# Kernel tuning notes

Hardware: AMD Instinct MI355X
Metric: run time of the kernel (lower is better)

The kernel has to match this reference:

```python
import jax, jax.numpy as jnp
import numpy as np

N = 128  # image size
J = 4    # number of scales
L = 4    # number of orientations


def make_morlet_filters(n, j_max, n_angles):
    """Fixed Morlet filter bank in Fourier space, shape [J, L, N, N] (real)."""
    freqs = np.fft.fftfreq(n) * 2.0 * np.pi
    kx = freqs[:, None] * np.ones((1, n))
    ky = np.ones((n, 1)) * freqs[None, :]
    filters = np.zeros((j_max, n_angles, n, n), dtype=np.float32)
    for j in range(j_max):
        k0 = 3.0 * np.pi / 4.0 / (2.0 ** j)   # central frequency of scale j
        sigma = 0.8 * (2.0 ** j)               # gaussian width in space
        for l in range(n_angles):
            theta = np.pi * l / n_angles
            k0x, k0y = k0 * np.cos(theta), k0 * np.sin(theta)
            beta = np.exp(-0.5 * sigma ** 2 * k0 ** 2)  # zero-mean correction
            g_shift = np.exp(-0.5 * sigma ** 2 * ((kx - k0x) ** 2 + (ky - k0y) ** 2))
            g_zero = np.exp(-0.5 * sigma ** 2 * (kx ** 2 + ky ** 2))
            filters[j, l] = g_shift - beta * g_zero
    return jnp.asarray(filters)


PSI = make_morlet_filters(N, J, L)  # fixed (non-learned) filter bank
VALID_PAIRS = [(j1, j2) for j1 in range(J) for j2 in range(J) if j2 > j1]  # 6 pairs


def setup_inputs() -> dict:
    key = jax.random.key(0)
    k1, k2, k3, k4, k5 = jax.random.split(key, 5)
    B = 64
    return {
        "image_batch": jax.random.normal(k1, (B, N, N), dtype=jnp.float32),
        "fc1_w": jax.random.normal(k2, (4, 11), dtype=jnp.float32) * 0.3,
        "fc1_b": jax.random.normal(k3, (4,), dtype=jnp.float32) * 0.1,
        "fc2_w": jax.random.normal(k4, (10, 4), dtype=jnp.float32) * 0.3,
        "fc2_b": jax.random.normal(k5, (10,), dtype=jnp.float32) * 0.1,
    }


def _scattering(image):
    # image: [B, N, N]
    i_hat = jnp.fft.fft2(image)  # [B,N,N] complex64
    s0 = jnp.mean(image, axis=(1, 2))  # [B]
    # first order: |x * psi_{j1,l1}|  -> [B,J,L,N,N]
    u1 = jnp.abs(jnp.fft.ifft2(i_hat[:, None, None] * PSI[None]))
    s1 = jnp.mean(u1, axis=(2, 3, 4))  # [B,J] averaged over orientations+space
    u1_hat = jnp.fft.fft2(u1)  # [B,J,L,N,N]
    # second order: only j2 > j1 (others NaN in original and masked out)
    s2_list = []
    for (j1, j2) in VALID_PAIRS:
        # [B, L1, L2, N, N]
        field = jnp.fft.ifft2(u1_hat[:, j1, :, None] * PSI[j2][None, None])
        s2_list.append(jnp.mean(jnp.abs(field), axis=(1, 2, 3, 4)))
    s2 = jnp.stack(s2_list, axis=1)  # [B,6]
    return jnp.concatenate([s0[:, None], s1, s2], axis=1)  # [B,11]


def reference(image_batch, fc1_w, fc1_b, fc2_w, fc2_b):
    coeffs = _scattering(image_batch)                      # [B,11]
    h = jax.nn.relu(coeffs @ fc1_w.T + fc1_b)              # [B,4]
    return jax.nn.sigmoid(h @ fc2_w.T + fc2_b)             # [B,10]
```

## Files before the change

### kernel.cpp

```cpp
#include <hip/hip_runtime.h>
#include <math.h>

#define NN   128
#define SS   129
#define TT   512
#define NPIX 16384
#define EPT  32
#define SG   65
#define SG32 33


__device__ __forceinline__ float2 cmul(float2 a, float2 w) {
    return make_float2(a.x * w.x - a.y * w.y, a.x * w.y + a.y * w.x);
}
__device__ __forceinline__ float2 cmulc(float2 a, float2 w) {
    return make_float2(a.x * w.x + a.y * w.y, a.y * w.x - a.x * w.y);
}

template<int SGN>
__device__ __forceinline__ void fft4(float2* f) {
    float2 t0 = make_float2(f[0].x + f[2].x, f[0].y + f[2].y);
    float2 t1 = make_float2(f[0].x - f[2].x, f[0].y - f[2].y);
    float2 t2 = make_float2(f[1].x + f[3].x, f[1].y + f[3].y);
    float2 t3 = make_float2(f[1].x - f[3].x, f[1].y - f[3].y);
    float2 t3i = (SGN > 0) ? make_float2(-t3.y, t3.x) : make_float2(t3.y, -t3.x);
    f[0] = make_float2(t0.x + t2.x, t0.y + t2.y);
    f[1] = make_float2(t1.x + t3i.x, t1.y + t3i.y);
    f[2] = make_float2(t0.x - t2.x, t0.y - t2.y);
    f[3] = make_float2(t1.x - t3i.x, t1.y - t3i.y);
}

template<int SGN>
__device__ __forceinline__ void fft8(float2* f) {
    const float R = 0.70710678118654752f;
    const float WC[4] = {1.f, R, 0.f, -R};
    const float WS[4] = {0.f, R, 1.f, R};
    #pragma unroll
    for (int stage = 0; stage < 3; ++stage) {
        const int L = 8 >> stage, half = L >> 1, step = 1 << stage;
        #pragma unroll
        for (int base = 0; base < 8; base += L) {
            #pragma unroll
            for (int j = 0; j < half; ++j) {
                float2 u = f[base + j], v = f[base + half + j];
                f[base + j] = make_float2(u.x + v.x, u.y + v.y);
                float dx = u.x - v.x, dy = u.y - v.y;
                const int t = j * step;
                const float wr = WC[t];
                const float wi = (SGN > 0) ? WS[t] : -WS[t];
                f[base + half + j] = make_float2(dx * wr - dy * wi, dx * wi + dy * wr);
            }
        }
    }
    float2 tmp;
    tmp = f[1]; f[1] = f[4]; f[4] = tmp;
    tmp = f[3]; f[3] = f[6]; f[6] = tmp;
}

template<int SGN>
__device__ __forceinline__ void fft16(float2* f) {
    const float WC[8] = {1.f, 0.92387953251f, 0.70710678119f, 0.38268343236f,
                         0.f, -0.38268343236f, -0.70710678119f, -0.92387953251f};
    const float WS[8] = {0.f, 0.38268343236f, 0.70710678119f, 0.92387953251f,
                         1.f, 0.92387953251f, 0.70710678119f, 0.38268343236f};
    #pragma unroll
    for (int stage = 0; stage < 4; ++stage) {
        const int L = 16 >> stage, half = L >> 1, step = 1 << stage;
        #pragma unroll
        for (int base = 0; base < 16; base += L) {
            #pragma unroll
            for (int j = 0; j < half; ++j) {
                float2 u = f[base + j], v = f[base + half + j];
                f[base + j] = make_float2(u.x + v.x, u.y + v.y);
                float dx = u.x - v.x, dy = u.y - v.y;
                const int t = j * step;
                const float wr = WC[t];
                const float wi = (SGN > 0) ? WS[t] : -WS[t];
                f[base + half + j] = make_float2(dx * wr - dy * wi, dx * wi + dy * wr);
            }
        }
    }
    float2 tmp;
    tmp = f[1];  f[1]  = f[8];  f[8]  = tmp;
    tmp = f[2];  f[2]  = f[4];  f[4]  = tmp;
    tmp = f[3];  f[3]  = f[12]; f[12] = tmp;
    tmp = f[5];  f[5]  = f[10]; f[10] = tmp;
    tmp = f[7];  f[7]  = f[14]; f[14] = tmp;
    tmp = f[11]; f[11] = f[13]; f[13] = tmp;
}

__device__ __forceinline__ float waveReduceSum(float v) {
    #pragma unroll
    for (int off = 32; off > 0; off >>= 1) v += __shfl_down(v, off, 64);
    return v;
}

__device__ __forceinline__ void buildTw(float2* tw, int tid) {
    if (tid < 128) {
        float s, c;
        __sincosf((float)tid * 0.04908738521234052f, &s, &c);
        tw[tid] = make_float2(c, s);
    }
}

__device__ __forceinline__ float pass32x4(float4* __restrict__ P4a,
                                          float4* __restrict__ P4b,
                                          const float2* __restrict__ tw, int tid) {
    __syncthreads();
    {
        float4* P = (tid & 256) ? P4b : P4a;
        int line = tid & 31, a = (tid >> 5) & 7;
        float2 f0[4], f1[4];
        #pragma unroll
        for (int kb = 0; kb < 4; ++kb) {
            float4 v = P[(4 * a + kb) * SG32 + line];
            f0[kb] = make_float2(v.x, v.y); f1[kb] = make_float2(v.z, v.w);
        }
        fft4<1>(f0); fft4<1>(f1);
        #pragma unroll
        for (int t = 0; t < 4; ++t) {
            float2 w = tw[4 * t * a];
            float2 aa = cmul(f0[t], w), d = cmul(f1[t], w);
            P[(4 * a + t) * SG32 + line] = make_float4(aa.x, aa.y, d.x, d.y);
        }
    }
    __syncthreads();
    if (tid < 256) {
        float4* P = (tid & 128) ? P4b : P4a;
        int line = tid & 31, t = (tid >> 5) & 3;
        float2 f0[8], f1[8];
        #pragma unroll
        for (int a = 0; a < 8; ++a) {
            float4 v = P[(4 * a + t) * SG32 + line];
            f0[a] = make_float2(v.x, v.y); f1[a] = make_float2(v.z, v.w);
        }
        fft8<1>(f0); fft8<1>(f1);
        #pragma unroll
        for (int n1 = 0; n1 < 8; ++n1)
            P[(4 * n1 + t) * SG32 + line] =
                make_float4(f0[n1].x, f0[n1].y, f1[n1].x, f1[n1].y);
    }
    __syncthreads();
    {
        float4* P = (tid & 256) ? P4b : P4a;
        int row = tid & 31, a = (tid >> 5) & 7;
        float4* R = P + row * SG32 + 4 * a;
        float2 f0[4], f1[4];
        #pragma unroll
        for (int kb = 0; kb < 4; ++kb) {
            float4 v = R[kb];
            f0[kb] = make_float2(v.x, v.y); f1[kb] = make_float2(v.z, v.w);
        }
        fft4<1>(f0); fft4<1>(f1);
        #pragma unroll
        for (int t = 0; t < 4; ++t) {
            float2 w = tw[4 * t * a];
            float2 aa = cmul(f0[t], w), d = cmul(f1[t], w);
            R[t] = make_float4(aa.x, aa.y, d.x, d.y);
        }
    }
    __syncthreads();
    float a2 = 0.f;
    if (tid < 256) {
        float4* P = (tid & 128) ? P4b : P4a;
        int row = tid & 31, t = (tid >> 5) & 3;
        float4* R = P + row * SG32 + t;
        float2 f0[8], f1[8];
        #pragma unroll
        for (int a = 0; a < 8; ++a) {
            float4 v = R[4 * a];
            f0[a] = make_float2(v.x, v.y); f1[a] = make_float2(v.z, v.w);
        }
        fft8<1>(f0); fft8<1>(f1);
        #pragma unroll
        for (int n1 = 0; n1 < 8; ++n1) {
            a2 += sqrtf(f0[n1].x * f0[n1].x + f0[n1].y * f0[n1].y);
            a2 += sqrtf(f1[n1].x * f1[n1].x + f1[n1].y * f1[n1].y);
        }
    }
    return a2;
}

__device__ __forceinline__ void pass32combo(float2* __restrict__ Q0, float2* __restrict__ Q1,
                                            float2* __restrict__ Q2, float2* __restrict__ Q3,
                                            float4* __restrict__ Pa, float4* __restrict__ Pb,
                                            const float2* __restrict__ tw, int tid,
                                            float& aq, float& ap) {
    __syncthreads();
    {
        float2* Qx = (tid & 256) ? Q2 : Q0;
        float2* Qy = (tid & 256) ? Q3 : Q1;
        float4* P  = (tid & 256) ? Pb : Pa;
        int line = tid & 31, a = (tid >> 5) & 7;
        float2 q0[4], q1[4], f0[4], f1[4];
        #pragma unroll
        for (int kb = 0; kb < 4; ++kb) {
            int o = (4 * a + kb) * SG32 + line;
            q0[kb] = Qx[o]; q1[kb] = Qy[o];
            float4 v = P[o];
            f0[kb] = make_float2(v.x, v.y); f1[kb] = make_float2(v.z, v.w);
        }
        fft4<1>(q0); fft4<1>(q1); fft4<1>(f0); fft4<1>(f1);
        #pragma unroll
        for (int t = 0; t < 4; ++t) {
            float2 w = tw[4 * t * a];
            int o = (4 * a + t) * SG32 + line;
            Qx[o] = cmul(q0[t], w); Qy[o] = cmul(q1[t], w);
            float2 aa = cmul(f0[t], w), d = cmul(f1[t], w);
            P[o] = make_float4(aa.x, aa.y, d.x, d.y);
        }
    }
    __syncthreads();
    if (tid < 256) {
        float2* Qx = (tid & 128) ? Q2 : Q0;
        float2* Qy = (tid & 128) ? Q3 : Q1;
        float4* P  = (tid & 128) ? Pb : Pa;
        int line = tid & 31, t = (tid >> 5) & 3;
        float2 q0[8], q1[8], f0[8], f1[8];
        #pragma unroll
        for (int a = 0; a < 8; ++a) {
            int o = (4 * a + t) * SG32 + line;
            q0[a] = Qx[o]; q1[a] = Qy[o];
            float4 v = P[o];
            f0[a] = make_float2(v.x, v.y); f1[a] = make_float2(v.z, v.w);
        }
        fft8<1>(q0); fft8<1>(q1); fft8<1>(f0); fft8<1>(f1);
        #pragma unroll
        for (int n1 = 0; n1 < 8; ++n1) {
            int o = (4 * n1 + t) * SG32 + line;
            Qx[o] = q0[n1]; Qy[o] = q1[n1];
            P[o] = make_float4(f0[n1].x, f0[n1].y, f1[n1].x, f1[n1].y);
        }
    }
    __syncthreads();
    {
        float2* Qx = (tid & 256) ? Q2 : Q0;
        float2* Qy = (tid & 256) ? Q3 : Q1;
        float4* P  = (tid & 256) ? Pb : Pa;
        int row = tid & 31, a = (tid >> 5) & 7;
        int base = row * SG32 + 4 * a;
        float2 q0[4], q1[4], f0[4], f1[4];
        #pragma unroll
        for (int kb = 0; kb < 4; ++kb) {
            q0[kb] = Qx[base + kb]; q1[kb] = Qy[base + kb];
            float4 v = P[base + kb];
            f0[kb] = make_float2(v.x, v.y); f1[kb] = make_float2(v.z, v.w);
        }
        fft4<1>(q0); fft4<1>(q1); fft4<1>(f0); fft4<1>(f1);
        #pragma unroll
        for (int t = 0; t < 4; ++t) {
            float2 w = tw[4 * t * a];
            Qx[base + t] = cmul(q0[t], w); Qy[base + t] = cmul(q1[t], w);
            float2 aa = cmul(f0[t], w), d = cmul(f1[t], w);
            P[base + t] = make_float4(aa.x, aa.y, d.x, d.y);
        }
    }
    __syncthreads();
    aq = 0.f; ap = 0.f;
    if (tid < 256) {
        float2* Qx = (tid & 128) ? Q2 : Q0;
        float2* Qy = (tid & 128) ? Q3 : Q1;
        float4* P  = (tid & 128) ? Pb : Pa;
        int row = tid & 31, t = (tid >> 5) & 3;
        int base = row * SG32 + t;
        float2 q0[8], q1[8], f0[8], f1[8];
        #pragma unroll
        for (int a = 0; a < 8; ++a) {
            int o = base + 4 * a;
            q0[a] = Qx[o]; q1[a] = Qy[o];
            float4 v = P[o];
            f0[a] = make_float2(v.x, v.y); f1[a] = make_float2(v.z, v.w);
        }
        fft8<1>(q0); fft8<1>(q1); fft8<1>(f0); fft8<1>(f1);
        #pragma unroll
        for (int n1 = 0; n1 < 8; ++n1) {
            aq += sqrtf(q0[n1].x * q0[n1].x + q0[n1].y * q0[n1].y);
            aq += sqrtf(q1[n1].x * q1[n1].x + q1[n1].y * q1[n1].y);
            ap += sqrtf(f0[n1].x * f0[n1].x + f0[n1].y * f0[n1].y);
            ap += sqrtf(f1[n1].x * f1[n1].x + f1[n1].y * f1[n1].y);
        }
    }
}

template<int ES, int LS>
__device__ __forceinline__ void fwdA(float2* __restrict__ F,
                                     const float2* __restrict__ tw, int tid) {
    #pragma unroll
    for (int i = 0; i < 4; ++i) {
        int u = i * TT + tid;
        int t = u >> 7, x = u & 127;
        float2* M = F + x * LS;
        float2 f[8];
        #pragma unroll
        for (int n1 = 0; n1 < 8; ++n1) f[n1] = M[(t + 16 * n1) * ES];
        fft8<-1>(f);
        #pragma unroll
        for (int ka = 0; ka < 8; ++ka)
            M[(t + 16 * ka) * ES] = cmulc(f[ka], tw[t * ka]);
    }
}

template<int ES, int LS>
__device__ __forceinline__ void fwdB(float2* __restrict__ F, int tid) {
    #pragma unroll
    for (int i = 0; i < 2; ++i) {
        int u = i * TT + tid;
        int ka = u >> 7, x = u & 127;
        float2* M = F + x * LS;
        float2 g[16];
        #pragma unroll
        for (int t = 0; t < 16; ++t) g[t] = M[(16 * ka + t) * ES];
        fft16<-1>(g);
        #pragma unroll
        for (int kb = 0; kb < 16; ++kb) M[(16 * ka + kb) * ES] = g[kb];
    }
}

__device__ __forceinline__ void fwdB_col_capture(const float2* __restrict__ F, int tid,
                                                 float2* __restrict__ uh) {
    #pragma unroll
    for (int i = 0; i < 2; ++i) {
        int u = i * TT + tid;
        int ka = u >> 7, c = u & 127;
        float2 g[16];
        #pragma unroll
        for (int t = 0; t < 16; ++t) g[t] = F[(16 * ka + t) * SS + c];
        fft16<-1>(g);
        #pragma unroll
        for (int kb = 0; kb < 16; ++kb) uh[i * 16 + kb] = g[kb];
    }
}

template<int ES, int LS>
__device__ __forceinline__ void invA(float2* __restrict__ F,
                                     const float2* __restrict__ tw, int tid) {
    #pragma unroll
    for (int i = 0; i < 2; ++i) {
        int u = i * TT + tid;
        int ka = u >> 7, x = u & 127;
        float2* M = F + x * LS;
        float2 g[16];
        #pragma unroll
        for (int kb = 0; kb < 16; ++kb) g[kb] = M[(16 * ka + kb) * ES];
        fft16<1>(g);
        #pragma unroll
        for (int t = 0; t < 16; ++t)
            M[(16 * ka + t) * ES] = cmul(g[t], tw[t * ka]);
    }
}

template<int ES, int LS>
__device__ __forceinline__ void invB(float2* __restrict__ F, int tid) {
    #pragma unroll
    for (int i = 0; i < 4; ++i) {
        int u = i * TT + tid;
        int t = u >> 7, x = u & 127;
        float2* M = F + x * LS;
        float2 f[8];
        #pragma unroll
        for (int ka = 0; ka < 8; ++ka) f[ka] = M[(16 * ka + t) * ES];
        fft8<1>(f);
        #pragma unroll
        for (int nh = 0; nh < 8; ++nh) M[(t + 16 * nh) * ES] = f[nh];
    }
}

__device__ __forceinline__ void invBmag_fwdA_row(float2* __restrict__ F,
                                                 const float2* __restrict__ tw,
                                                 int tid, float& acc) {
    #pragma unroll
    for (int i = 0; i < 4; ++i) {
        int u = i * TT + tid;
        int t = u >> 7, x = u & 127;
        float2* M = F + x * SS;
        float2 f[8];
        #pragma unroll
        for (int ka = 0; ka < 8; ++ka) f[ka] = M[16 * ka + t];
        fft8<1>(f);
        #pragma unroll
        for (int nh = 0; nh < 8; ++nh) {
            float m = sqrtf(f[nh].x * f[nh].x + f[nh].y * f[nh].y);
            acc += m;
            f[nh] = make_float2(m, 0.f);
        }
        fft8<-1>(f);
        #pragma unroll
        for (int ka = 0; ka < 8; ++ka)
            M[t + 16 * ka] = cmulc(f[ka], tw[t * ka]);
    }
}

__global__ __attribute__((amdgpu_flat_work_group_size(TT, TT), amdgpu_waves_per_eu(4, 4)))
void k_pre1(const float* __restrict__ img,
            float* __restrict__ psi,
            float2* __restrict__ interm,
            float* __restrict__ coeffs) {
    __shared__ __align__(16) float2 F[32 * SS];
    __shared__ float2 tw[128];
    int blk = blockIdx.x, tid = threadIdx.x;
    if (blk >= 256) {
        if (blk == 384) {
            for (int i = tid; i < 64 * 11; i += TT) coeffs[i] = 0.f;
            return;
        }
        int fb = blk - 256;
        int f = fb >> 3, chunk = fb & 7;
        int j = f >> 2, l = f & 3;
        float k0    = 2.35619449019234493f / (float)(1 << j);
        float sigma = 0.8f * (float)(1 << j);
        float s2    = sigma * sigma;
        float theta = 0.78539816339744831f * (float)l;
        float k0x = k0 * cosf(theta);
        float k0y = k0 * sinf(theta);
        float beta = expf(-0.5f * s2 * k0 * k0);
        const float FSTEP = 0.04908738521234052f;
        float* dst = psi + (size_t)f * NPIX;
        int i0 = chunk * 2048, i1 = i0 + 2048;
        for (int i = i0 + tid; i < i1; i += TT) {
            int pr = i >> 7, pc = i & 127;
            int kr = (pr >> 4) + 8 * (pr & 15);
            int kc = (pc >> 4) + 8 * (pc & 15);
            float fr = (float)(kr < 64 ? kr : kr - 128) * FSTEP;
            float fc = (float)(kc < 64 ? kc : kc - 128) * FSTEP;
            float dx = fr - k0x, dy = fc - k0y;
            float g1 = expf(-0.5f * s2 * (dx * dx + dy * dy));
            float g0 = expf(-0.5f * s2 * (fr * fr + fc * fc));
            dst[i] = g1 - beta * g0;
        }
        return;
    }
    int b = blk >> 2, q = blk & 3;
    buildTw(tw, tid);
    const float* im = img + (size_t)b * NPIX + (size_t)q * 32 * NN;
    #pragma unroll
    for (int k = 0; k < 8; ++k) {
        int e = k * TT + tid;
        F[(e >> 7) * SS + (e & 127)] = make_float2(im[e], 0.f);
    }
    __syncthreads();
    {
        int x = tid & 31, t = tid >> 5;
        float2* M = F + x * SS;
        float2 f[8];
        #pragma unroll
        for (int n1 = 0; n1 < 8; ++n1) f[n1] = M[t + 16 * n1];
        fft8<-1>(f);
        #pragma unroll
        for (int ka = 0; ka < 8; ++ka)
            M[t + 16 * ka] = cmulc(f[ka], tw[t * ka]);
    }
    __syncthreads();
    if (tid < 256) {
        int x = tid & 31, ka = tid >> 5;
        float2* M = F + x * SS + 16 * ka;
        float2 g[16];
        #pragma unroll
        for (int t = 0; t < 16; ++t) g[t] = M[t];
        fft16<-1>(g);
        #pragma unroll
        for (int kb = 0; kb < 16; ++kb) M[kb] = g[kb];
    }
    __syncthreads();
    float2* dst = interm + (size_t)b * NPIX + (size_t)q * 32 * NN;
    #pragma unroll
    for (int k = 0; k < 8; ++k) {
        int e = k * TT + tid;
        dst[e] = F[(e >> 7) * SS + (e & 127)];
    }
}

__global__ __attribute__((amdgpu_flat_work_group_size(TT, TT), amdgpu_waves_per_eu(4, 4)))
void k_pre2(float2* __restrict__ ihat,
            float* __restrict__ coeffs) {
    __shared__ __align__(16) float2 F[128 * 33];
    __shared__ float2 tw[128];
    int blk = blockIdx.x, tid = threadIdx.x;
    int b = blk >> 2, q = blk & 3;
    buildTw(tw, tid);
    float2* base = ihat + (size_t)b * NPIX + q * 32;
    #pragma unroll
    for (int k = 0; k < 8; ++k) {
        int e = k * TT + tid;
        int r = e >> 5, cl = e & 31;
        F[r * 33 + cl] = base[r * NN + cl];
    }
    __syncthreads();
    {
        int cl = tid & 31, t = tid >> 5;
        float2 f[8];
        #pragma unroll
        for (int n1 = 0; n1 < 8; ++n1) f[n1] = F[(t + 16 * n1) * 33 + cl];
        fft8<-1>(f);
        #pragma unroll
        for (int ka = 0; ka < 8; ++ka)
            F[(t + 16 * ka) * 33 + cl] = cmulc(f[ka], tw[t * ka]);
    }
    __syncthreads();
    if (tid < 256) {
        int cl = tid & 31, ka = tid >> 5;
        float2 g[16];
        #pragma unroll
        for (int t = 0; t < 16; ++t) g[t] = F[(16 * ka + t) * 33 + cl];
        fft16<-1>(g);
        float2* dst = base + cl;
        #pragma unroll
        for (int kb = 0; kb < 16; ++kb)
            dst[(16 * ka + kb) * NN] = g[kb];
        if (q == 0 && cl == 0 && ka == 0)
            coeffs[b * 11 + 0] = g[0].x * (1.f / 16384.f);
    }
}

__global__ __attribute__((amdgpu_flat_work_group_size(TT, TT), amdgpu_waves_per_eu(2, 2)))
void k_scat_big(const float2* __restrict__ ihat,
                const float* __restrict__ psi,
                float* __restrict__ coeffs) {
    __shared__ __align__(16) float2 F[16640];
    __shared__ float2 tw[128];
    float4* G4a = (float4*)F;
    float4* G4b = (float4*)(F + 8320);
    float2* G2a = F;
    float2* G2b = F + 4160;
    float2* G2c = F + 8320;
    float2* G2d = F + 12480;
    float4* P4a = (float4*)F;
    float4* P4b = (float4*)F + 1056;
    int tid = threadIdx.x;
    int x = blockIdx.x;
    int b = x & 63, l1 = x >> 6;
    const float2* ih = ihat + (size_t)b * NPIX;
    const float*  p1 = psi + (size_t)l1 * NPIX;
    buildTw(tw, tid);

    const float S1_128 = 9.3132257461547852e-10f;
    const float S2TR   = 5.6843418860808015e-14f;
    const float S2_03  = 2.2737367544323206e-13f;

    int kalo = tid >> 7, c = tid & 127;
    {
        #pragma unroll
        for (int i = 0; i < 2; ++i) {
            int ka = kalo + 4 * i;
            float2 g[16];
            #pragma unroll
            for (int kb = 0; kb < 16; ++kb) {
                int e = (16 * ka + kb) * NN + c;
                float2 z = ih[e];
                float  p = p1[e];
                g[kb] = make_float2(z.x * p, z.y * p);
            }
            fft16<1>(g);
            #pragma unroll
            for (int t = 0; t < 16; ++t)
                F[(16 * ka + t) * SS + c] = cmul(g[t], tw[t * ka]);
        }
    }
    __syncthreads();
    invB<SS, 1>(F, tid);      __syncthreads();
    invA<1, SS>(F, tw, tid);  __syncthreads();
    float acc = 0.f;
    invBmag_fwdA_row(F, tw, tid, acc);
    float ws1 = waveReduceSum(acc);
    if ((tid & 63) == 0) atomicAdd(&coeffs[b * 11 + 1], ws1 * S1_128);
    __syncthreads();
    fwdB<1, SS>(F, tid);      __syncthreads();
    fwdA<SS, 1>(F, tw, tid);  __syncthreads();
    float2 uh[32];
    fwdB_col_capture(F, tid, uh);
    __syncthreads();

    int m = c & 15;
    bool colKeep = (m < 4) || (m >= 12);
    int pc64 = 8 * (c >> 4) + ((m < 4) ? m : (m - 8));
    int fc = (c >> 4) + 8 * (c & 15);

    {
        const int ORW[4] = {21, 15, 0, -15};
        const int OCW[4] = { 0, 15, 21,  15};
        bool ckw[4]; int pcw[4];
        #pragma unroll
        for (int w = 0; w < 4; ++w) {
            int dc = (fc - OCW[w]) & 127;
            ckw[w] = (dc < 32) || (dc >= 96);
            int uc = (dc < 32) ? dc : (dc - 64);
            pcw[w] = 8 * (uc & 7) + (uc >> 3);
        }
        #pragma unroll
        for (int i = 0; i < 2; ++i) {
            int ka = kalo + 4 * i;
            #pragma unroll
            for (int kb = 0; kb < 16; ++kb) {
                int fr = ka + 8 * kb;
                float2 z = uh[i * 16 + kb];
                int e = (16 * ka + kb) * NN + c;
                #pragma unroll
                for (int w = 0; w < 4; ++w) {
                    if (ckw[w]) {
                        int dr = (fr - ORW[w]) & 127;
                        if (dr < 32 || dr >= 96) {
                            int ur = (dr < 32) ? dr : (dr - 64);
                            int pr = 8 * (ur & 7) + (ur >> 3);
                            float pv = psi[(size_t)(4 + w) * NPIX + e];
                            float2* G = (w == 0) ? G2a : (w == 1) ? G2b
                                       : (w == 2) ? G2c : G2d;
                            G[pr * SG + pcw[w]] = make_float2(z.x * pv, z.y * pv);
                        }
                    }
                }
            }
        }
        __syncthreads();
        {
            int col = tid & 63, k8 = tid >> 6;
            float2 f0[8], f1[8], f2[8], f3[8];
            #pragma unroll
            for (int kb = 0; kb < 8; ++kb) {
                int o = (8 * k8 + kb) * SG + col;
                f0[kb] = G2a[o]; f1[kb] = G2b[o]; f2[kb] = G2c[o]; f3[kb] = G2d[o];
            }
            fft8<1>(f0); fft8<1>(f1); fft8<1>(f2); fft8<1>(f3);
            #pragma unroll
            for (int q = 0; q < 8; ++q) {
                float2 w = tw[2 * q * k8];
                int o = (8 * k8 + q) * SG + col;
                G2a[o] = cmul(f0[q], w); G2b[o] = cmul(f1[q], w);
                G2c[o] = cmul(f2[q], w); G2d[o] = cmul(f3[q], w);
            }
        }
        __syncthreads();
        {
            int col = tid & 63, q = tid >> 6;
            float2 f0[8], f1[8], f2[8], f3[8];
            #pragma unroll
            for (int k8 = 0; k8 < 8; ++k8) {
                int o = (8 * k8 + q) * SG + col;
                f0[k8] = G2a[o]; f1[k8] = G2b[o]; f2[k8] = G2c[o]; f3[k8] = G2d[o];
            }
            fft8<1>(f0); fft8<1>(f1); fft8<1>(f2); fft8<1>(f3);
            #pragma unroll
            for (int n1 = 0; n1 < 8; ++n1) {
                int o = (8 * n1 + q) * SG + col;
                G2a[o] = f0[n1]; G2b[o] = f1[n1]; G2c[o] = f2[n1]; G2d[o] = f3[n1];
            }
        }
        __syncthreads();
        {
            int row = tid & 63, k8 = tid >> 6;
            int base = row * SG + 8 * k8;
            float2 f0[8], f1[8], f2[8], f3[8];
            #pragma unroll
            for (int kb = 0; kb < 8; ++kb) {
                f0[kb] = G2a[base + kb]; f1[kb] = G2b[base + kb];
                f2[kb] = G2c[base + kb]; f3[kb] = G2d[base + kb];
            }
            fft8<1>(f0); fft8<1>(f1); fft8<1>(f2); fft8<1>(f3);
            #pragma unroll
            for (int q = 0; q < 8; ++q) {
                float2 w = tw[2 * q * k8];
                G2a[base + q] = cmul(f0[q], w); G2b[base + q] = cmul(f1[q], w);
                G2c[base + q] = cmul(f2[q], w); G2d[base + q] = cmul(f3[q], w);
            }
        }
        __syncthreads();
        float a2 = 0.f;
        {
            int row = tid & 63, q = tid >> 6;
            int base = row * SG + q;
            float2 f0[8], f1[8], f2[8], f3[8];
            #pragma unroll
            for (int k8 = 0; k8 < 8; ++k8) {
                int o = base + 8 * k8;
                f0[k8] = G2a[o]; f1[k8] = G2b[o]; f2[k8] = G2c[o]; f3[k8] = G2d[o];
            }
            fft8<1>(f0); fft8<1>(f1); fft8<1>(f2); fft8<1>(f3);
            #pragma unroll
            for (int n1 = 0; n1 < 8; ++n1) {
                a2 += sqrtf(f0[n1].x * f0[n1].x + f0[n1].y * f0[n1].y);
                a2 += sqrtf(f1[n1].x * f1[n1].x + f1[n1].y * f1[n1].y);
                a2 += sqrtf(f2[n1].x * f2[n1].x + f2[n1].y * f2[n1].y);
                a2 += sqrtf(f3[n1].x * f3[n1].x + f3[n1].y * f3[n1].y);
            }
        }
        float ws2 = waveReduceSum(a2);
        if ((tid & 63) == 0) atomicAdd(&coeffs[b * 11 + 5 + 0], ws2 * S2TR);
        __syncthreads();
    }

    {
        const float* p0 = psi + (size_t)8 * NPIX;
        const float* pq1 = p0 + NPIX;
        const float* pq2 = pq1 + NPIX;
        const float* pq3 = pq2 + NPIX;
        if (colKeep) {
            #pragma unroll
            for (int i = 0; i < 2; ++i) {
                int ka = kalo + 4 * i;
                #pragma unroll
                for (int kb = 0; kb < 16; ++kb) {
                    if (kb < 4 || kb >= 12) {
                        int pr64 = 8 * ka + ((kb < 4) ? kb : (kb - 8));
                        float2 z = uh[i * 16 + kb];
                        int e = (16 * ka + kb) * NN + c;
                        float a0 = p0[e], a1 = pq1[e], a2f = pq2[e], a3 = pq3[e];
                        G4a[pr64 * SG + pc64] =
                            make_float4(z.x * a0, z.y * a0, z.x * a1, z.y * a1);
                        G4b[pr64 * SG + pc64] =
                            make_float4(z.x * a2f, z.y * a2f, z.x * a3, z.y * a3);
                    }
                }
            }
        }
        __syncthreads();
        {
            int col = tid & 63, k8 = tid >> 6;
            float2 f0[8], f1[8], f2[8], f3[8];
            #pragma unroll
            for (int kb = 0; kb < 8; ++kb) {
                int o = (8 * k8 + kb) * SG + col;
                float4 v = G4a[o];
                f0[kb] = make_float2(v.x, v.y); f1[kb] = make_float2(v.z, v.w);
                float4 u = G4b[o];
                f2[kb] = make_float2(u.x, u.y); f3[kb] = make_float2(u.z, u.w);
            }
            fft8<1>(f0); fft8<1>(f1); fft8<1>(f2); fft8<1>(f3);
            #pragma unroll
            for (int q = 0; q < 8; ++q) {
                float2 w = tw[2 * q * k8];
                int o = (8 * k8 + q) * SG + col;
                float2 a = cmul(f0[q], w), d = cmul(f1[q], w);
                G4a[o] = make_float4(a.x, a.y, d.x, d.y);
                float2 a2c = cmul(f2[q], w), d2 = cmul(f3[q], w);
                G4b[o] = make_float4(a2c.x, a2c.y, d2.x, d2.y);
            }
        }
        __syncthreads();
        {
            int col = tid & 63, q = tid >> 6;
            float2 f0[8], f1[8], f2[8], f3[8];
            #pragma unroll
            for (int k8 = 0; k8 < 8; ++k8) {
                int o = (8 * k8 + q) * SG + col;
                float4 v = G4a[o];
                f0[k8] = make_float2(v.x, v.y); f1[k8] = make_float2(v.z, v.w);
                float4 u = G4b[o];
                f2[k8] = make_float2(u.x, u.y); f3[k8] = make_float2(u.z, u.w);
            }
            fft8<1>(f0); fft8<1>(f1); fft8<1>(f2); fft8<1>(f3);
            #pragma unroll
            for (int n1 = 0; n1 < 8; ++n1) {
                int o = (8 * n1 + q) * SG + col;
                G4a[o] = make_float4(f0[n1].x, f0[n1].y, f1[n1].x, f1[n1].y);
                G4b[o] = make_float4(f2[n1].x, f2[n1].y, f3[n1].x, f3[n1].y);
            }
        }
        __syncthreads();
        {
            int row = tid & 63, k8 = tid >> 6;
            int base = row * SG + 8 * k8;
            float2 f0[8], f1[8], f2[8], f3[8];
            #pragma unroll
            for (int kb = 0; kb < 8; ++kb) {
                float4 v = G4a[base + kb];
                f0[kb] = make_float2(v.x, v.y); f1[kb] = make_float2(v.z, v.w);
                float4 u = G4b[base + kb];
                f2[kb] = make_float2(u.x, u.y); f3[kb] = make_float2(u.z, u.w);
            }
            fft8<1>(f0); fft8<1>(f1); fft8<1>(f2); fft8<1>(f3);
            #pragma unroll
            for (int q = 0; q < 8; ++q) {
                float2 w = tw[2 * q * k8];
                float2 a = cmul(f0[q], w), d = cmul(f1[q], w);
                G4a[base + q] = make_float4(a.x, a.y, d.x, d.y);
                float2 a2c = cmul(f2[q], w), d2 = cmul(f3[q], w);
                G4b[base + q] = make_float4(a2c.x, a2c.y, d2.x, d2.y);
            }
        }
        __syncthreads();
        float a2 = 0.f;
        {
            int row = tid & 63, q = tid >> 6;
            int base = row * SG + q;
            float2 f0[8], f1[8], f2[8], f3[8];
            #pragma unroll
            for (int k8 = 0; k8 < 8; ++k8) {
                float4 v = G4a[base + 8 * k8];
                f0[k8] = make_float2(v.x, v.y); f1[k8] = make_float2(v.z, v.w);
                float4 u = G4b[base + 8 * k8];
                f2[k8] = make_float2(u.x, u.y); f3[k8] = make_float2(u.z, u.w);
            }
            fft8<1>(f0); fft8<1>(f1); fft8<1>(f2); fft8<1>(f3);
            #pragma unroll
            for (int n1 = 0; n1 < 8; ++n1) {
                a2 += sqrtf(f0[n1].x * f0[n1].x + f0[n1].y * f0[n1].y);
                a2 += sqrtf(f1[n1].x * f1[n1].x + f1[n1].y * f1[n1].y);
                a2 += sqrtf(f2[n1].x * f2[n1].x + f2[n1].y * f2[n1].y);
                a2 += sqrtf(f3[n1].x * f3[n1].x + f3[n1].y * f3[n1].y);
            }
        }
        float ws2 = waveReduceSum(a2);
        if ((tid & 63) == 0) atomicAdd(&coeffs[b * 11 + 5 + 1], ws2 * S2TR);
        __syncthreads();
    }

    {
        bool ck32 = (m < 2) || (m >= 14);
        int pc32 = 4 * (c >> 4) + ((m < 2) ? m : (m - 12));
        const float* p0 = psi + (size_t)12 * NPIX;
        const float* pq1 = p0 + NPIX;
        const float* pq2 = pq1 + NPIX;
        const float* pq3 = pq2 + NPIX;
        if (ck32) {
            #pragma unroll
            for (int i = 0; i < 2; ++i) {
                int ka = kalo + 4 * i;
                #pragma unroll
                for (int kb = 0; kb < 16; ++kb) {
                    if (kb < 2 || kb >= 14) {
                        int pr32 = 4 * ka + ((kb < 2) ? kb : (kb - 12));
                        float2 z = uh[i * 16 + kb];
                        int e = (16 * ka + kb) * NN + c;
                        float a0 = p0[e], a1 = pq1[e], a2f = pq2[e], a3 = pq3[e];
                        P4a[pr32 * SG32 + pc32] =
                            make_float4(z.x * a0, z.y * a0, z.x * a1, z.y * a1);
                        P4b[pr32 * SG32 + pc32] =
                            make_float4(z.x * a2f, z.y * a2f, z.x * a3, z.y * a3);
                    }
                }
            }
        }
        float a2 = pass32x4(P4a, P4b, tw, tid);
        float ws2 = waveReduceSum(a2);
        if ((tid & 63) == 0) atomicAdd(&coeffs[b * 11 + 5 + 2], ws2 * S2_03);
    }
}

__global__ __attribute__((amdgpu_flat_work_group_size(TT, TT), amdgpu_waves_per_eu(4, 4)))
void k_scat_small(const float2* __restrict__ ihat,
                  const float* __restrict__ psi,
                  float* __restrict__ coeffs) {
    __shared__ __align__(16) float2 S[8448];
    __shared__ float2 tw[128];
    float2* G2  = S;
    float2* G32 = S;
    float2* Qs0 = S;
    float2* Qs1 = S + 1056;
    float2* Qs2 = S + 2112;
    float2* Qs3 = S + 3168;
    float4* Psa = (float4*)(S + 4224);
    float4* Psb = (float4*)(S + 6336);
    int tid = threadIdx.x;
    int x = blockIdx.x;
    int b = x & 63, l1 = (x >> 6) & 3;
    int t0 = x >> 8;
    const float2* ih = ihat + (size_t)b * NPIX;
    const float*  p1 = psi + (size_t)(((t0 == 0) ? 1 : (t0 + 1)) * 4 + l1) * NPIX;
    buildTw(tw, tid);

    const float S1_64 = 3.7252902984619141e-9f;
    const float S1_32 = 1.4901161193847656e-8f;
    const float S2_32 = 9.0949470177292824e-13f;

    int kalo = tid >> 7, c = tid & 127;

    if (t0 == 0) {
        const int OR1[4] = {21, 15, 0, -15};
        const int OC1[4] = { 0, 15, 21,  15};
        int fc = (c >> 4) + 8 * (c & 15);
        int dc = (fc - OC1[l1]) & 127;
        bool ck = (dc < 32) || (dc >= 96);
        int ucw = (dc < 32) ? dc : (dc - 64);
        int pcd = 8 * (ucw & 7) + (ucw >> 3);
        if (ck) {
            #pragma unroll
            for (int i = 0; i < 2; ++i) {
                int ka = kalo + 4 * i;
                #pragma unroll
                for (int kb = 0; kb < 16; ++kb) {
                    int fr = ka + 8 * kb;
                    int dr = (fr - OR1[l1]) & 127;
                    if (dr < 32 || dr >= 96) {
                        int ur = (dr < 32) ? dr : (dr - 64);
                        int pr = 8 * (ur & 7) + (ur >> 3);
                        int e = (16 * ka + kb) * NN + c;
                        float2 z = ih[e];
                        float  p = p1[e];
                        G2[pr * SG + pcd] = make_float2(z.x * p, z.y * p);
                    }
                }
            }
        }
        __syncthreads();
        {
            int col = tid & 63, k8 = tid >> 6;
            float2 f[8];
            #pragma unroll
            for (int kb = 0; kb < 8; ++kb) f[kb] = G2[(8 * k8 + kb) * SG + col];
            fft8<1>(f);
            #pragma unroll
            for (int q = 0; q < 8; ++q)
                G2[(8 * k8 + q) * SG + col] = cmul(f[q], tw[2 * q * k8]);
        }
        __syncthreads();
        {
            int col = tid & 63, q = tid >> 6;
            float2 f[8];
            #pragma unroll
            for (int k8 = 0; k8 < 8; ++k8) f[k8] = G2[(8 * k8 + q) * SG + col];
            fft8<1>(f);
            #pragma unroll
            for (int n1 = 0; n1 < 8; ++n1) G2[(8 * n1 + q) * SG + col] = f[n1];
        }
        __syncthreads();
        {
            int row = tid & 63, k8 = tid >> 6;
            float2* R = G2 + row * SG + 8 * k8;
            float2 f[8];
            #pragma unroll
            for (int kb = 0; kb < 8; ++kb) f[kb] = R[kb];
            fft8<1>(f);
            #pragma unroll
            for (int q = 0; q < 8; ++q) R[q] = cmul(f[q], tw[2 * q * k8]);
        }
        __syncthreads();
        float acc = 0.f;
        {
            int row = tid & 63, q = tid >> 6;
            float2* R = G2 + row * SG + q;
            float2 f[8];
            #pragma unroll
            for (int k8 = 0; k8 < 8; ++k8) f[k8] = R[8 * k8];
            fft8<1>(f);
            #pragma unroll
            for (int n1 = 0; n1 < 8; ++n1) {
                float mg = sqrtf(f[n1].x * f[n1].x + f[n1].y * f[n1].y);
                acc += mg;
                f[n1] = make_float2(mg, 0.f);
            }
            fft8<-1>(f);
            #pragma unroll
            for (int ka = 0; ka < 8; ++ka)
                R[8 * ka] = cmulc(f[ka], tw[2 * q * ka]);
        }
        float ws1 = waveReduceSum(acc);
        if ((tid & 63) == 0) atomicAdd(&coeffs[b * 11 + 2], ws1 * S1_64);
        __syncthreads();
        {
            int row2 = tid & 63, ka = tid >> 6;
            float2* R2 = G2 + row2 * SG + 8 * ka;
            float2 g[8];
            #pragma unroll
            for (int t = 0; t < 8; ++t) g[t] = R2[t];
            fft8<-1>(g);
            #pragma unroll
            for (int kb = 0; kb < 8; ++kb) R2[kb] = g[kb];
        }
        __syncthreads();
        {
            int col = tid & 63, t = tid >> 6;
            float2 g[8];
            #pragma unroll
            for (int n1 = 0; n1 < 8; ++n1) g[n1] = G2[(t + 8 * n1) * SG + col];
            fft8<-1>(g);
            #pragma unroll
            for (int ka = 0; ka < 8; ++ka)
                G2[(t + 8 * ka) * SG + col] = cmulc(g[ka], tw[2 * t * ka]);
        }
        __syncthreads();
        float2 vh[8];
        int c6 = tid & 63, ka8 = tid >> 6;
        {
            float2 g[8];
            #pragma unroll
            for (int t = 0; t < 8; ++t) g[t] = G2[(8 * ka8 + t) * SG + c6];
            fft8<-1>(g);
            #pragma unroll
            for (int kb = 0; kb < 8; ++kb) vh[kb] = g[kb];
        }
        __syncthreads();

        int uc64 = 8 * (c6 & 7) + (c6 >> 3);
        int fc128 = (uc64 < 32) ? uc64 : (uc64 + 64);
        int scI = 16 * (fc128 & 7) + (fc128 >> 3);
        int se[8];
        #pragma unroll
        for (int kb = 0; kb < 8; ++kb) {
            int ur = 8 * kb + ka8;
            int fr128 = (ur < 32) ? ur : (ur + 64);
            se[kb] = (16 * (fr128 & 7) + (fr128 >> 3)) * NN + scI;
        }

        {
            const int OR2[4] = {9, 6, 0, -6};
            const int OC2[4] = {0, 6, 9,  6};
            bool ckq[4]; int pcq[4];
            #pragma unroll
            for (int w = 0; w < 4; ++w) {
                int dcw = (uc64 - OC2[w]) & 63;
                ckq[w] = (dcw < 16) || (dcw >= 48);
                int f32c = (dcw < 16) ? dcw : (dcw - 32);
                pcq[w] = 4 * (f32c & 7) + (f32c >> 3);
            }
            int m6 = c6 & 7;
            bool ckV = (m6 < 2) || (m6 >= 6);
            int p32c = 4 * (c6 >> 3) + ((m6 < 2) ? m6 : (m6 - 4));
            const float* p30 = psi + (size_t)12 * NPIX;
            #pragma unroll
            for (int kb = 0; kb < 8; ++kb) {
                int ur = 8 * kb + ka8;
                float2 z = vh[kb];
                int e = se[kb];
                #pragma unroll
                for (int w = 0; w < 4; ++w) {
                    if (ckq[w]) {
                        int dr = (ur - OR2[w]) & 63;
                        if (dr < 16 || dr >= 48) {
                            int f32r = (dr < 16) ? dr : (dr - 32);
                            int pr = 4 * (f32r & 7) + (f32r >> 3);
                            float pv = psi[(size_t)(8 + w) * NPIX + e];
                            float2* Q = (w == 0) ? Qs0 : (w == 1) ? Qs1
                                       : (w == 2) ? Qs2 : Qs3;
                            Q[pr * SG32 + pcq[w]] = make_float2(z.x * pv, z.y * pv);
                        }
                    }
                }
                if (ckV && (kb < 2 || kb >= 6)) {
                    int pr32 = 4 * ka8 + (kb & 3);
                    float a0 = p30[e], a1 = p30[NPIX + e];
                    float a2f = p30[2 * NPIX + e], a3 = p30[3 * NPIX + e];
                    Psa[pr32 * SG32 + p32c] =
                        make_float4(z.x * a0, z.y * a0, z.x * a1, z.y * a1);
                    Psb[pr32 * SG32 + p32c] =
                        make_float4(z.x * a2f, z.y * a2f, z.x * a3, z.y * a3);
                }
            }
            float aq, ap;
            pass32combo(Qs0, Qs1, Qs2, Qs3, Psa, Psb, tw, tid, aq, ap);
            float wsq = waveReduceSum(aq);
            float wsp = waveReduceSum(ap);
            if ((tid & 63) == 0) {
                atomicAdd(&coeffs[b * 11 + 5 + 3], wsq * S2_32);
                atomicAdd(&coeffs[b * 11 + 5 + 4], wsp * S2_32);
            }
        }
        return;
    }

    if (t0 == 2) {
        int m = c & 15;
        bool ck32 = (m < 2) || (m >= 14);
        int pc32 = 4 * (c >> 4) + ((m < 2) ? m : (m - 12));
        if (ck32) {
            #pragma unroll
            for (int i = 0; i < 2; ++i) {
                int ka = kalo + 4 * i;
                #pragma unroll
                for (int kb = 0; kb < 16; ++kb) {
                    if (kb < 2 || kb >= 14) {
                        int e = (16 * ka + kb) * NN + c;
                        float2 z = ih[e];
                        float  p = p1[e];
                        int pr32 = 4 * ka + ((kb < 2) ? kb : (kb - 12));
                        G32[pr32 * SG32 + pc32] = make_float2(z.x * p, z.y * p);
                    }
                }
            }
        }
        __syncthreads();
        if (tid < 256) {
            int line = tid & 31, a = tid >> 5;
            float2 f[4];
            #pragma unroll
            for (int kb = 0; kb < 4; ++kb) f[kb] = G32[(4 * a + kb) * SG32 + line];
            fft4<1>(f);
            #pragma unroll
            for (int t = 0; t < 4; ++t)
                G32[(4 * a + t) * SG32 + line] = cmul(f[t], tw[4 * t * a]);
        }
        __syncthreads();
        if (tid < 128) {
            int line = tid & 31, t = tid >> 5;
            float2 f[8];
            #pragma unroll
            for (int a = 0; a < 8; ++a) f[a] = G32[(4 * a + t) * SG32 + line];
            fft8<1>(f);
            #pragma unroll
            for (int n1 = 0; n1 < 8; ++n1) G32[(4 * n1 + t) * SG32 + line] = f[n1];
        }
        __syncthreads();
        if (tid < 256) {
            int row = tid & 31, a = tid >> 5;
            float2* R = G32 + row * SG32 + 4 * a;
            float2 f[4];
            #pragma unroll
            for (int kb = 0; kb < 4; ++kb) f[kb] = R[kb];
            fft4<1>(f);
            #pragma unroll
            for (int t = 0; t < 4; ++t) R[t] = cmul(f[t], tw[4 * t * a]);
        }
        __syncthreads();
        float acc = 0.f;
        if (tid < 128) {
            int row = tid & 31, t = tid >> 5;
            float2* R = G32 + row * SG32 + t;
            float2 f[8];
            #pragma unroll
            for (int a = 0; a < 8; ++a) f[a] = R[4 * a];
            fft8<1>(f);
            #pragma unroll
            for (int n1 = 0; n1 < 8; ++n1)
                acc += sqrtf(f[n1].x * f[n1].x + f[n1].y * f[n1].y);
        }
        float ws1 = waveReduceSum(acc);
        if ((tid & 63) == 0 && tid < 128) atomicAdd(&coeffs[b * 11 + 4], ws1 * S1_32);
        return;
    }

    {
        const float S2_23 = 3.6379788070917130e-12f;
        const int OR1[4] = {9, 6, 0, -6};
        const int OC1[4] = {0, 6, 9,  6};
        float2* G = S;
        float4* Pa = (float4*)(S + 1088);
        float4* Pb = (float4*)(S + 3200);
        int fc = (c >> 4) + 8 * (c & 15);
        int dc = (fc - OC1[l1]) & 127;
        bool ck = (dc < 16) || (dc >= 112);
        int f32c = (dc < 16) ? dc : (dc - 96);
        int pcd = 4 * (f32c & 7) + (f32c >> 3);
        if (ck) {
            #pragma unroll
            for (int i = 0; i < 2; ++i) {
                int ka = kalo + 4 * i;
                #pragma unroll
                for (int kb = 0; kb < 16; ++kb) {
                    int fr = ka + 8 * kb;
                    int dr = (fr - OR1[l1]) & 127;
                    if (dr < 16 || dr >= 112) {
                        int f32r = (dr < 16) ? dr : (dr - 96);
                        int pr = 4 * (f32r & 7) + (f32r >> 3);
                        int e = (16 * ka + kb) * NN + c;
                        float2 z = ih[e];
                        float  p = p1[e];
                        G[pr * SG32 + pcd] = make_float2(z.x * p, z.y * p);
                    }
                }
            }
        }
        __syncthreads();
        if (tid < 256) {
            int line = tid & 31, a = tid >> 5;
            float2 f[4];
            #pragma unroll
            for (int kb = 0; kb < 4; ++kb) f[kb] = G[(4 * a + kb) * SG32 + line];
            fft4<1>(f);
            #pragma unroll
            for (int t = 0; t < 4; ++t)
                G[(4 * a + t) * SG32 + line] = cmul(f[t], tw[4 * t * a]);
        }
        __syncthreads();
        if (tid < 128) {
            int line = tid & 31, t = tid >> 5;
            float2 f[8];
            #pragma unroll
            for (int a = 0; a < 8; ++a) f[a] = G[(4 * a + t) * SG32 + line];
            fft8<1>(f);
            #pragma unroll
            for (int n1 = 0; n1 < 8; ++n1) G[(4 * n1 + t) * SG32 + line] = f[n1];
        }
        __syncthreads();
        if (tid < 256) {
            int row = tid & 31, a = tid >> 5;
            float2* R = G + row * SG32 + 4 * a;
            float2 f[4];
            #pragma unroll
            for (int kb = 0; kb < 4; ++kb) f[kb] = R[kb];
            fft4<1>(f);
            #pragma unroll
            for (int t = 0; t < 4; ++t) R[t] = cmul(f[t], tw[4 * t * a]);
        }
        __syncthreads();
        float acc = 0.f;
        if (tid < 128) {
            int row = tid & 31, t = tid >> 5;
            float2* R = G + row * SG32 + t;
            float2 f[8];
            #pragma unroll
            for (int a = 0; a < 8; ++a) f[a] = R[4 * a];
            fft8<1>(f);
            #pragma unroll
            for (int n1 = 0; n1 < 8; ++n1) {
                float mg = sqrtf(f[n1].x * f[n1].x + f[n1].y * f[n1].y);
                acc += mg;
                R[4 * n1] = make_float2(mg, 0.f);
            }
        }
        float ws1 = waveReduceSum(acc);
        if ((tid & 63) == 0 && tid < 128) atomicAdd(&coeffs[b * 11 + 3], ws1 * S1_32);
        __syncthreads();
        if (tid < 256) {
            int row = tid & 31, a = tid >> 5;
            float2* R = G + row * SG32 + 4 * a;
            float2 f[4];
            #pragma unroll
            for (int kb = 0; kb < 4; ++kb) f[kb] = R[kb];
            fft4<-1>(f);
            #pragma unroll
            for (int t = 0; t < 4; ++t) R[t] = cmulc(f[t], tw[4 * t * a]);
        }
        __syncthreads();
        if (tid < 128) {
            int row = tid & 31, t = tid >> 5;
            float2* R = G + row * SG32 + t;
            float2 f[8];
            #pragma unroll
            for (int a = 0; a < 8; ++a) f[a] = R[4 * a];
            fft8<-1>(f);
            #pragma unroll
            for (int n1 = 0; n1 < 8; ++n1) R[4 * n1] = f[n1];
        }
        __syncthreads();
        if (tid < 256) {
            int line = tid & 31, a = tid >> 5;
            float2 f[4];
            #pragma unroll
            for (int kb = 0; kb < 4; ++kb) f[kb] = G[(4 * a + kb) * SG32 + line];
            fft4<-1>(f);
            #pragma unroll
            for (int t = 0; t < 4; ++t)
                G[(4 * a + t) * SG32 + line] = cmulc(f[t], tw[4 * t * a]);
        }
        __syncthreads();
        if (tid < 128) {
            int line = tid & 31, t = tid >> 5;
            float2 f[8];
            #pragma unroll
            for (int a = 0; a < 8; ++a) f[a] = G[(4 * a + t) * SG32 + line];
            fft8<-1>(f);
            #pragma unroll
            for (int n1 = 0; n1 < 8; ++n1) G[(4 * n1 + t) * SG32 + line] = f[n1];
        }
        __syncthreads();
        {
            const float* q0 = psi + (size_t)12 * NPIX;
            const float* q1 = q0 + NPIX;
            const float* q2 = q1 + NPIX;
            const float* q3 = q2 + NPIX;
            #pragma unroll
            for (int ii = 0; ii < 2; ++ii) {
                int s = ii * 512 + tid;
                int pr = s >> 5, pc = s & 31;
                int ur = (pr >> 2) + 8 * (pr & 3);
                int uc = (pc >> 2) + 8 * (pc & 3);
                int fr = (ur < 16) ? ur : (ur + 96);
                int fcc = (uc < 16) ? uc : (uc + 96);
                int e = (16 * (fr & 7) + (fr >> 3)) * NN
                      + 16 * (fcc & 7) + (fcc >> 3);
                float2 z = G[pr * SG32 + pc];
                float a0 = q0[e], a1 = q1[e], a2f = q2[e], a3 = q3[e];
                Pa[pr * SG32 + pc] = make_float4(z.x * a0, z.y * a0, z.x * a1, z.y * a1);
                Pb[pr * SG32 + pc] = make_float4(z.x * a2f, z.y * a2f, z.x * a3, z.y * a3);
            }
        }
        float a2 = pass32x4(Pa, Pb, tw, tid);
        float ws2 = waveReduceSum(a2);
        if ((tid & 63) == 0) atomicAdd(&coeffs[b * 11 + 5 + 5], ws2 * S2_23);
    }
}

__global__ void k_mlp(const float* __restrict__ coeffs,
                      const float* __restrict__ w1, const float* __restrict__ b1,
                      const float* __restrict__ w2, const float* __restrict__ b2,
                      float* __restrict__ out) {
    int b = threadIdx.x;
    if (b >= 64) return;
    float c[11];
    #pragma unroll
    for (int i = 0; i < 11; ++i) c[i] = coeffs[b * 11 + i];
    float h[4];
    #pragma unroll
    for (int k = 0; k < 4; ++k) {
        float s = b1[k];
        #pragma unroll
        for (int i = 0; i < 11; ++i) s += w1[k * 11 + i] * c[i];
        h[k] = fmaxf(s, 0.f);
    }
    #pragma unroll
    for (int o = 0; o < 10; ++o) {
        float s = b2[o];
        #pragma unroll
        for (int k = 0; k < 4; ++k) s += w2[o * 4 + k] * h[k];
        out[b * 10 + o] = 1.f / (1.f + expf(-s));
    }
}

extern "C" void kernel_launch(void* const* d_in, const int* in_sizes, int n_in,
                              void* d_out, int out_size, void* d_ws, size_t ws_size,
                              hipStream_t stream) {
    const float* img = (const float*)d_in[0];
    const float* w1  = (const float*)d_in[1];
    const float* b1  = (const float*)d_in[2];
    const float* w2  = (const float*)d_in[3];
    const float* b2  = (const float*)d_in[4];
    float* out = (float*)d_out;

    float*  ws     = (float*)d_ws;
    float*  psi    = ws;
    float2* ihat   = (float2*)(ws + 16 * NPIX);
    float*  coeffs = ws + 16 * NPIX + 2 * 64 * NPIX;

    hipLaunchKernelGGL(k_pre1,       dim3(385), dim3(TT), 0, stream, img, psi, ihat, coeffs);
    hipLaunchKernelGGL(k_pre2,       dim3(256), dim3(TT), 0, stream, ihat, coeffs);
    hipLaunchKernelGGL(k_scat_big,   dim3(256), dim3(TT), 0, stream, ihat, psi, coeffs);
    hipLaunchKernelGGL(k_scat_small, dim3(768), dim3(TT), 0, stream, ihat, psi, coeffs);
    hipLaunchKernelGGL(k_mlp,        dim3(1),   dim3(64), 0, stream, coeffs, w1, b1, w2, b2, out);
}
```

Baseline: 168.4 us.

## Compute j1=0 second-order pairs with shifted 32x32 band windows instead of 64x64 FFTs

Replaces the 64x64 inverse FFT path for the (j1=0, j2=2) pair with a 32x32 path. For each orientation it gathers a shifted 32x32 window around the filter's passband from a staged 64x64 spectrum copy, then runs it through a combined 32-point pass that shares work with the (j1=0, j2=3) pair. This cuts FFT size, shared-memory traffic and barriers in the large-block kernel. In exchange it relies on the j2=2 filters being effectively confined to those windows, which changes accuracy slightly, and it uses more complex index arithmetic in the gather.

```diff
diff --git a/kernel.cpp b/kernel.cpp
--- a/kernel.cpp
+++ b/kernel.cpp
@@ -517,14 +517,17 @@
                 float* __restrict__ coeffs) {
     __shared__ __align__(16) float2 F[16640];
     __shared__ float2 tw[128];
-    float4* G4a = (float4*)F;
-    float4* G4b = (float4*)(F + 8320);
     float2* G2a = F;
     float2* G2b = F + 4160;
     float2* G2c = F + 8320;
     float2* G2d = F + 12480;
-    float4* P4a = (float4*)F;
-    float4* P4b = (float4*)F + 1056;
+    float2* Q0 = F;
+    float2* Q1 = F + 1056;
+    float2* Q2 = F + 2112;
+    float2* Q3 = F + 3168;
+    float4* Pa = (float4*)(F + 4224);
+    float4* Pb = (float4*)(F + 6336);
+    float2* H  = F + 8448;
     int tid = threadIdx.x;
     int x = blockIdx.x;
     int b = x & 63, l1 = x >> 6;
@@ -686,151 +689,68 @@
         __syncthreads();
     }
 
+    if (colKeep) {
+        #pragma unroll
+        for (int i = 0; i < 2; ++i) {
+            int ka = kalo + 4 * i;
+            #pragma unroll
+            for (int kb = 0; kb < 16; ++kb) {
+                if (kb < 4 || kb >= 12) {
+                    int pr64 = 8 * ka + ((kb < 4) ? kb : (kb - 8));
+                    H[pr64 * 64 + pc64] = uh[i * 16 + kb];
+                }
+            }
+        }
+    }
+    __syncthreads();
+
     {
-        const float* p0 = psi + (size_t)8 * NPIX;
-        const float* pq1 = p0 + NPIX;
-        const float* pq2 = pq1 + NPIX;
-        const float* pq3 = pq2 + NPIX;
-        if (colKeep) {
-            #pragma unroll
-            for (int i = 0; i < 2; ++i) {
-                int ka = kalo + 4 * i;
-                #pragma unroll
-                for (int kb = 0; kb < 16; ++kb) {
-                    if (kb < 4 || kb >= 12) {
-                        int pr64 = 8 * ka + ((kb < 4) ? kb : (kb - 8));
-                        float2 z = uh[i * 16 + kb];
-                        int e = (16 * ka + kb) * NN + c;
-                        float a0 = p0[e], a1 = pq1[e], a2f = pq2[e], a3 = pq3[e];
-                        G4a[pr64 * SG + pc64] =
-                            make_float4(z.x * a0, z.y * a0, z.x * a1, z.y * a1);
-                        G4b[pr64 * SG + pc64] =
-                            make_float4(z.x * a2f, z.y * a2f, z.x * a3, z.y * a3);
-                    }
-                }
-            }
-        }
-        __syncthreads();
-        {
-            int col = tid & 63, k8 = tid >> 6;
-            float2 f0[8], f1[8], f2[8], f3[8];
-            #pragma unroll
-            for (int kb = 0; kb < 8; ++kb) {
-                int o = (8 * k8 + kb) * SG + col;
-                float4 v = G4a[o];
-                f0[kb] = make_float2(v.x, v.y); f1[kb] = make_float2(v.z, v.w);
-                float4 u = G4b[o];
-                f2[kb] = make_float2(u.x, u.y); f3[kb] = make_float2(u.z, u.w);
-            }
-            fft8<1>(f0); fft8<1>(f1); fft8<1>(f2); fft8<1>(f3);
-            #pragma unroll
-            for (int q = 0; q < 8; ++q) {
-                float2 w = tw[2 * q * k8];
-                int o = (8 * k8 + q) * SG + col;
-                float2 a = cmul(f0[q], w), d = cmul(f1[q], w);
-                G4a[o] = make_float4(a.x, a.y, d.x, d.y);
-                float2 a2c = cmul(f2[q], w), d2 = cmul(f3[q], w);
-                G4b[o] = make_float4(a2c.x, a2c.y, d2.x, d2.y);
-            }
-        }
-        __syncthreads();
-        {
-            int col = tid & 63, q = tid >> 6;
-            float2 f0[8], f1[8], f2[8], f3[8];
-            #pragma unroll
-            for (int k8 = 0; k8 < 8; ++k8) {
-                int o = (8 * k8 + q) * SG + col;
-                float4 v = G4a[o];
-                f0[k8] = make_float2(v.x, v.y); f1[k8] = make_float2(v.z, v.w);
-                float4 u = G4b[o];
-                f2[k8] = make_float2(u.x, u.y); f3[k8] = make_float2(u.z, u.w);
-            }
-            fft8<1>(f0); fft8<1>(f1); fft8<1>(f2); fft8<1>(f3);
-            #pragma unroll
-            for (int n1 = 0; n1 < 8; ++n1) {
-                int o = (8 * n1 + q) * SG + col;
-                G4a[o] = make_float4(f0[n1].x, f0[n1].y, f1[n1].x, f1[n1].y);
-                G4b[o] = make_float4(f2[n1].x, f2[n1].y, f3[n1].x, f3[n1].y);
-            }
-        }
-        __syncthreads();
-        {
-            int row = tid & 63, k8 = tid >> 6;
-            int base = row * SG + 8 * k8;
-            float2 f0[8], f1[8], f2[8], f3[8];
-            #pragma unroll
-            for (int kb = 0; kb < 8; ++kb) {
-                float4 v = G4a[base + kb];
-                f0[kb] = make_float2(v.x, v.y); f1[kb] = make_float2(v.z, v.w);
-                float4 u = G4b[base + kb];
-                f2[kb] = make_float2(u.x, u.y); f3[kb] = make_float2(u.z, u.w);
-            }
-            fft8<1>(f0); fft8<1>(f1); fft8<1>(f2); fft8<1>(f3);
-            #pragma unroll
-            for (int q = 0; q < 8; ++q) {
-                float2 w = tw[2 * q * k8];
-                float2 a = cmul(f0[q], w), d = cmul(f1[q], w);
-                G4a[base + q] = make_float4(a.x, a.y, d.x, d.y);
-                float2 a2c = cmul(f2[q], w), d2 = cmul(f3[q], w);
-                G4b[base + q] = make_float4(a2c.x, a2c.y, d2.x, d2.y);
-            }
-        }
-        __syncthreads();
-        float a2 = 0.f;
-        {
-            int row = tid & 63, q = tid >> 6;
-            int base = row * SG + q;
-            float2 f0[8], f1[8], f2[8], f3[8];
-            #pragma unroll
-            for (int k8 = 0; k8 < 8; ++k8) {
-                float4 v = G4a[base + 8 * k8];
-                f0[k8] = make_float2(v.x, v.y); f1[k8] = make_float2(v.z, v.w);
-                float4 u = G4b[base + 8 * k8];
-                f2[k8] = make_float2(u.x, u.y); f3[k8] = make_float2(u.z, u.w);
-            }
-            fft8<1>(f0); fft8<1>(f1); fft8<1>(f2); fft8<1>(f3);
-            #pragma unroll
-            for (int n1 = 0; n1 < 8; ++n1) {
-                a2 += sqrtf(f0[n1].x * f0[n1].x + f0[n1].y * f0[n1].y);
-                a2 += sqrtf(f1[n1].x * f1[n1].x + f1[n1].y * f1[n1].y);
-                a2 += sqrtf(f2[n1].x * f2[n1].x + f2[n1].y * f2[n1].y);
-                a2 += sqrtf(f3[n1].x * f3[n1].x + f3[n1].y * f3[n1].y);
-            }
-        }
-        float ws2 = waveReduceSum(a2);
-        if ((tid & 63) == 0) atomicAdd(&coeffs[b * 11 + 5 + 1], ws2 * S2TR);
-        __syncthreads();
-    }
-
-    {
-        bool ck32 = (m < 2) || (m >= 14);
-        int pc32 = 4 * (c >> 4) + ((m < 2) ? m : (m - 12));
-        const float* p0 = psi + (size_t)12 * NPIX;
-        const float* pq1 = p0 + NPIX;
-        const float* pq2 = pq1 + NPIX;
-        const float* pq3 = pq2 + NPIX;
-        if (ck32) {
-            #pragma unroll
-            for (int i = 0; i < 2; ++i) {
-                int ka = kalo + 4 * i;
-                #pragma unroll
-                for (int kb = 0; kb < 16; ++kb) {
-                    if (kb < 2 || kb >= 14) {
-                        int pr32 = 4 * ka + ((kb < 2) ? kb : (kb - 12));
-                        float2 z = uh[i * 16 + kb];
-                        int e = (16 * ka + kb) * NN + c;
-                        float a0 = p0[e], a1 = pq1[e], a2f = pq2[e], a3 = pq3[e];
-                        P4a[pr32 * SG32 + pc32] =
-                            make_float4(z.x * a0, z.y * a0, z.x * a1, z.y * a1);
-                        P4b[pr32 * SG32 + pc32] =
-                            make_float4(z.x * a2f, z.y * a2f, z.x * a3, z.y * a3);
-                    }
-                }
-            }
-        }
-        float a2 = pass32x4(P4a, P4b, tw, tid);
-        float ws2 = waveReduceSum(a2);
-        if ((tid & 63) == 0) atomicAdd(&coeffs[b * 11 + 5 + 2], ws2 * S2_03);
+        const int OR2[4] = {9, 6, 0, -6};
+        const int OC2[4] = {0, 6, 9,  6};
+        const float* p20 = psi + (size_t)8 * NPIX;
+        const float* p30 = psi + (size_t)12 * NPIX;
+        #pragma unroll
+        for (int ii = 0; ii < 2; ++ii) {
+            int s = ii * 512 + tid;
+            int pr = s >> 5, pc = s & 31;
+            int u32r = (pr >> 2) + 8 * (pr & 3);
+            int u32c = (pc >> 2) + 8 * (pc & 3);
+            int drs = (u32r < 16) ? u32r : (u32r - 32);
+            int dcs = (u32c < 16) ? u32c : (u32c - 32);
+            {
+                int fr = drs & 127, fcc = dcs & 127;
+                int hr = 8 * (fr & 7) + (fr >> 3) - ((fr >= 96) ? 8 : 0);
+                int hc = 8 * (fcc & 7) + (fcc >> 3) - ((fcc >= 96) ? 8 : 0);
+                float2 z = H[hr * 64 + hc];
+                int e = (16 * (fr & 7) + (fr >> 3)) * NN
+                      + 16 * (fcc & 7) + (fcc >> 3);
+                float a0 = p30[e], a1 = p30[NPIX + e];
+                float a2f = p30[2 * NPIX + e], a3 = p30[3 * NPIX + e];
+                Pa[pr * SG32 + pc] = make_float4(z.x * a0, z.y * a0, z.x * a1, z.y * a1);
+                Pb[pr * SG32 + pc] = make_float4(z.x * a2f, z.y * a2f, z.x * a3, z.y * a3);
+            }
+            #pragma unroll
+            for (int w = 0; w < 4; ++w) {
+                int fr = (drs + OR2[w]) & 127;
+                int fcc = (dcs + OC2[w]) & 127;
+                int hr = 8 * (fr & 7) + (fr >> 3) - ((fr >= 96) ? 8 : 0);
+                int hc = 8 * (fcc & 7) + (fcc >> 3) - ((fcc >= 96) ? 8 : 0);
+                float2 z = H[hr * 64 + hc];
+                int e = (16 * (fr & 7) + (fr >> 3)) * NN
+                      + 16 * (fcc & 7) + (fcc >> 3);
+                float pv = p20[(size_t)w * NPIX + e];
+                float2* Q = (w == 0) ? Q0 : (w == 1) ? Q1 : (w == 2) ? Q2 : Q3;
+                Q[pr * SG32 + pc] = make_float2(z.x * pv, z.y * pv);
+            }
+        }
+        float aq, ap;
+        pass32combo(Q0, Q1, Q2, Q3, Pa, Pb, tw, tid, aq, ap);
+        float wsq = waveReduceSum(aq);
+        float wsp = waveReduceSum(ap);
+        if ((tid & 63) == 0) {
+            atomicAdd(&coeffs[b * 11 + 5 + 1], wsq * S2_03);
+            atomicAdd(&coeffs[b * 11 + 5 + 2], wsp * S2_03);
+        }
     }
 }
 
```

Result: slower. 265.8 us (+57.9%).
